# Kernel optimization log

Measured on AMD Instinct MI355X. Metric: run time of the kernel, lower is better.

Reference implementation:

```python
import jax, jax.numpy as jnp
import numpy as np
import math

EMBED_DIM = 512
NUM_HEADS = 8
HEAD_DIM = EMBED_DIM // NUM_HEADS


def setup_inputs() -> dict:
    key = jax.random.key(0)
    ks = jax.random.split(key, 11)
    s = 1.0 / math.sqrt(EMBED_DIM)
    x = jax.random.normal(ks[0], (8, EMBED_DIM, 32, 32), dtype=jnp.float32)
    Wq = jax.random.uniform(ks[1], (EMBED_DIM, EMBED_DIM), jnp.float32, -s, s)
    bq = jax.random.uniform(ks[2], (EMBED_DIM,), jnp.float32, -s, s)
    Wk = jax.random.uniform(ks[3], (EMBED_DIM, EMBED_DIM), jnp.float32, -s, s)
    bk = jax.random.uniform(ks[4], (EMBED_DIM,), jnp.float32, -s, s)
    Wv = jax.random.uniform(ks[5], (EMBED_DIM, EMBED_DIM), jnp.float32, -s, s)
    bv = jax.random.uniform(ks[6], (EMBED_DIM,), jnp.float32, -s, s)
    Wo = jax.random.uniform(ks[7], (EMBED_DIM, EMBED_DIM), jnp.float32, -s, s)
    bo = jax.random.uniform(ks[8], (EMBED_DIM,), jnp.float32, -s, s)
    gamma = jnp.ones((EMBED_DIM,), jnp.float32)
    beta = jnp.zeros((EMBED_DIM,), jnp.float32)
    return {"x": x, "Wq": Wq, "bq": bq, "Wk": Wk, "bk": bk, "Wv": Wv,
            "bv": bv, "Wo": Wo, "bo": bo, "gamma": gamma, "beta": beta}


def layer_norm(x, gamma, beta, eps=1e-5):
    mu = jnp.mean(x, axis=-1, keepdims=True)
    var = jnp.mean(jnp.square(x - mu), axis=-1, keepdims=True)
    return (x - mu) * jax.lax.rsqrt(var + eps) * gamma + beta


def reference(x, Wq, bq, Wk, bk, Wv, bv, Wo, bo, gamma, beta):
    B, C, H, W = x.shape
    S = H * W
    # [B, S, C]
    x_flat = x.reshape(B, C, S).transpose(0, 2, 1)
    residual = x_flat
    xn = layer_norm(x_flat, gamma, beta)
    # torch Linear: y = x @ W^T + b
    q = (xn @ Wq.T + bq).reshape(B, S, NUM_HEADS, HEAD_DIM)
    k = (xn @ Wk.T + bk).reshape(B, S, NUM_HEADS, HEAD_DIM)
    v = (xn @ Wv.T + bv).reshape(B, S, NUM_HEADS, HEAD_DIM)
    scale = 1.0 / math.sqrt(HEAD_DIM)
    scores = jnp.einsum('bqhd,bkhd->bhqk', q, k) * scale
    attn = jax.nn.softmax(scores, axis=-1)  # dropout is identity in eval
    out = jnp.einsum('bhqk,bkhd->bqhd', attn, v).reshape(B, S, C)
    out = out @ Wo.T + bo + residual
    return out.transpose(0, 2, 1).reshape(B, C, H, W)
```

## Files before the change

### kernel.cpp

```cpp
#include <hip/hip_runtime.h>
#include <hip/hip_bf16.h>

typedef __bf16 bf16_t;
typedef __bf16 bf16x8 __attribute__((ext_vector_type(8)));
typedef float floatx4 __attribute__((ext_vector_type(4)));

#define EMBED 512
#define S_LEN 1024
#define NH 8
#define HD 64
#define LDK 1056
#define LDV 1088

#define MFMA16(a, b, c) __builtin_amdgcn_mfma_f32_16x16x32_bf16(a, b, c, 0, 0, 0)

static __device__ __forceinline__ bf16_t f2bf(float f) {
    unsigned int x = __builtin_bit_cast(unsigned int, f);
    unsigned int lsb = (x >> 16) & 1u;
    x += 0x7fffu + lsb;
    unsigned short u = (unsigned short)(x >> 16);
    return __builtin_bit_cast(bf16_t, u);
}
static __device__ __forceinline__ float bf2f(bf16_t v) {
    unsigned short u = __builtin_bit_cast(unsigned short, v);
    unsigned int x = ((unsigned int)u) << 16;
    return __builtin_bit_cast(float, x);
}
static __device__ __forceinline__ unsigned int pack2(float lo, float hi) {
    return (__builtin_bit_cast(unsigned int, lo) >> 16) |
           (__builtin_bit_cast(unsigned int, hi) & 0xFFFF0000u);
}
static __device__ __forceinline__ unsigned int pack2r(float lo, float hi) {
    unsigned short a = __builtin_bit_cast(unsigned short, f2bf(lo));
    unsigned short b = __builtin_bit_cast(unsigned short, f2bf(hi));
    return (unsigned int)a | ((unsigned int)b << 16);
}

__global__ __launch_bounds__(256) void cvt4_kernel(const float* __restrict__ s0,
                                                   const float* __restrict__ s1,
                                                   const float* __restrict__ s2,
                                                   const float* __restrict__ s3,
                                                   bf16_t* __restrict__ d0,
                                                   bf16_t* __restrict__ d1,
                                                   bf16_t* __restrict__ d2,
                                                   bf16_t* __restrict__ d3) {
    const float* s; bf16_t* d;
    switch (blockIdx.y) {
        case 0:  s = s0; d = d0; break;
        case 1:  s = s1; d = d1; break;
        case 2:  s = s2; d = d2; break;
        default: s = s3; d = d3; break;
    }
    int i = (blockIdx.x * 256 + threadIdx.x) * 8;
#pragma unroll
    for (int j = 0; j < 8; ++j) d[i + j] = f2bf(s[i + j]);
}

__global__ __launch_bounds__(256) void ln_fused_kernel(const float* __restrict__ x,
                                                       const float* __restrict__ gamma,
                                                       const float* __restrict__ beta,
                                                       bf16_t* __restrict__ xn) {
    __shared__ float T[32][521];
    __shared__ float Pm[32][33], Pq[32][33];
    __shared__ float Mu[32], Rs[32];
    int bid = blockIdx.x;
    int b = bid >> 5, s0 = (bid & 31) * 32;
    int t = threadIdx.x;
    int lc = t >> 3;
    int si = (t & 7) * 4;
    const float* xp = x + ((size_t)b * EMBED + lc) * S_LEN + s0 + si;
    float sm[4] = {}, sq[4] = {};
#pragma unroll
    for (int p = 0; p < 16; ++p) {
        int c = lc + p * 32;
        float4 v = *(const float4*)(xp + (size_t)p * 32 * S_LEN);
        int cs = c ^ ((c >> 3) & 0x38);
        T[si + 0][cs] = v.x; T[si + 1][cs] = v.y;
        T[si + 2][cs] = v.z; T[si + 3][cs] = v.w;
        sm[0] += v.x; sq[0] += v.x * v.x;
        sm[1] += v.y; sq[1] += v.y * v.y;
        sm[2] += v.z; sq[2] += v.z * v.z;
        sm[3] += v.w; sq[3] += v.w * v.w;
    }
#pragma unroll
    for (int k = 0; k < 4; ++k) { Pm[si + k][lc] = sm[k]; Pq[si + k][lc] = sq[k]; }
    __syncthreads();
    if (t < 32) {
        float m = 0.f, q = 0.f;
#pragma unroll
        for (int j = 0; j < 32; ++j) { m += Pm[t][j]; q += Pq[t][j]; }
        float mu = m * (1.0f / EMBED);
        float var = q * (1.0f / EMBED) - mu * mu;
        Mu[t] = mu; Rs[t] = rsqrtf(var + 1e-5f);
    }
    __syncthreads();
    int cidx = t & 31;
    int rw = t >> 5;
#pragma unroll
    for (int rg = 0; rg < 4; ++rg) {
        int srl = rg * 8 + rw;
        float mu = Mu[srl], rs = Rs[srl];
        int cb = cidx * 16;
        bf16_t* dst = xn + ((size_t)b * S_LEN + s0 + srl) * EMBED + cb;
#pragma unroll
        for (int h = 0; h < 2; ++h) {
            int c0h = cb + h * 8;
            float4 g0 = *(const float4*)(gamma + c0h);
            float4 g1 = *(const float4*)(gamma + c0h + 4);
            float4 be0 = *(const float4*)(beta + c0h);
            float4 be1 = *(const float4*)(beta + c0h + 4);
            float gv[8] = {g0.x, g0.y, g0.z, g0.w, g1.x, g1.y, g1.z, g1.w};
            float bv[8] = {be0.x, be0.y, be0.z, be0.w, be1.x, be1.y, be1.z, be1.w};
            bf16x8 o;
#pragma unroll
            for (int j = 0; j < 8; ++j) {
                int c = c0h + j;
                int cs = c ^ ((c >> 3) & 0x38);
                o[j] = f2bf((T[srl][cs] - mu) * rs * gv[j] + bv[j]);
            }
            *(bf16x8*)(dst + h * 8) = o;
        }
    }
}

__global__ __launch_bounds__(256) void gemm_kernel(const bf16_t* __restrict__ X,
                                                   const bf16_t* __restrict__ W,
                                                   const float* __restrict__ b0,
                                                   const float* __restrict__ b1,
                                                   const float* __restrict__ b2,
                                                   bf16_t* __restrict__ Y,
                                                   bf16_t* __restrict__ vtb) {
    __shared__ __align__(16) bf16_t Wl[2][128 * 72];
    int t = threadIdx.x;
    int col0 = blockIdx.y * 128, row0 = blockIdx.x * 128;
    int scol = t >> 1, sseg = (t & 1) * 32;
    const bf16_t* wsrc = W + (size_t)(col0 + scol) * EMBED + sseg;
    {
        bf16x8 r0 = *(const bf16x8*)(wsrc);
        bf16x8 r1 = *(const bf16x8*)(wsrc + 8);
        bf16x8 r2 = *(const bf16x8*)(wsrc + 16);
        bf16x8 r3 = *(const bf16x8*)(wsrc + 24);
        bf16_t* d = &Wl[0][scol * 72 + sseg];
        *(bf16x8*)d = r0;        *(bf16x8*)(d + 8) = r1;
        *(bf16x8*)(d + 16) = r2; *(bf16x8*)(d + 24) = r3;
    }
    int lane = t & 63, w = t >> 6, g = lane >> 4, n16 = lane & 15;
    int rw0 = row0 + w * 32;
    const bf16_t* xr0 = X + (size_t)(rw0 + n16) * EMBED + g * 8;
    const bf16_t* xr1 = xr0 + (size_t)16 * EMBED;
    bf16x8 a00 = *(const bf16x8*)(xr0);
    bf16x8 a01 = *(const bf16x8*)(xr0 + 32);
    bf16x8 a10 = *(const bf16x8*)(xr1);
    bf16x8 a11 = *(const bf16x8*)(xr1 + 32);
    __syncthreads();
    floatx4 acc[2][8] = {};
#pragma unroll
    for (int kc = 0; kc < 8; ++kc) {
        bf16x8 p0, p1, p2, p3, na00, na01, na10, na11;
        if (kc < 7) {
            int ko = (kc + 1) * 64;
            p0 = *(const bf16x8*)(wsrc + ko);
            p1 = *(const bf16x8*)(wsrc + ko + 8);
            p2 = *(const bf16x8*)(wsrc + ko + 16);
            p3 = *(const bf16x8*)(wsrc + ko + 24);
            na00 = *(const bf16x8*)(xr0 + ko);
            na01 = *(const bf16x8*)(xr0 + ko + 32);
            na10 = *(const bf16x8*)(xr1 + ko);
            na11 = *(const bf16x8*)(xr1 + ko + 32);
        }
        const bf16_t* wl = &Wl[kc & 1][0];
#pragma unroll
        for (int kk = 0; kk < 2; ++kk) {
            bf16x8 s0 = (kk == 0) ? a00 : a01;
            bf16x8 s1 = (kk == 0) ? a10 : a11;
#pragma unroll
            for (int nt = 0; nt < 8; ++nt) {
                bf16x8 bfr = *(const bf16x8*)(&wl[(nt * 16 + n16) * 72 + kk * 32 + g * 8]);
                acc[0][nt] = MFMA16(s0, bfr, acc[0][nt]);
                acc[1][nt] = MFMA16(s1, bfr, acc[1][nt]);
            }
        }
        if (kc < 7) {
            bf16_t* d = &Wl[(kc + 1) & 1][scol * 72 + sseg];
            *(bf16x8*)d = p0;        *(bf16x8*)(d + 8) = p1;
            *(bf16x8*)(d + 16) = p2; *(bf16x8*)(d + 24) = p3;
            a00 = na00; a01 = na01; a10 = na10; a11 = na11;
        }
        __syncthreads();
    }
    if (col0 < 1024) {
        const float* bp = (col0 < 512) ? b0 : b1;
#pragma unroll
        for (int ar = 0; ar < 2; ++ar)
#pragma unroll
            for (int nt = 0; nt < 8; ++nt) {
                int col = col0 + nt * 16 + n16;
                float bv = bp[col & 511];
#pragma unroll
                for (int r = 0; r < 4; ++r) {
                    int row = rw0 + ar * 16 + g * 4 + r;
                    Y[(size_t)row * LDK + col] = f2bf(acc[ar][nt][r] + bv);
                }
            }
    } else {
        bf16_t* Tl = &Wl[0][0];
#pragma unroll
        for (int ar = 0; ar < 2; ++ar)
#pragma unroll
            for (int nt = 0; nt < 8; ++nt) {
                int chl = nt * 16 + n16;
                float bv = b2[(col0 & 511) + chl];
                uint2 pr;
                pr.x = pack2r(acc[ar][nt][0] + bv, acc[ar][nt][1] + bv);
                pr.y = pack2r(acc[ar][nt][2] + bv, acc[ar][nt][3] + bv);
                *(uint2*)(&Tl[chl * 136 + w * 32 + ar * 16 + g * 4]) = pr;
            }
        __syncthreads();
        int ch = t >> 1, seg = (t & 1) * 64;
        int bb = row0 >> 10, s0 = row0 & 1023;
        bf16_t* dst = vtb + ((size_t)(bb * EMBED + (col0 - 1024) + ch)) * LDV + s0 + seg;
        const bf16_t* srcl = &Tl[ch * 136 + seg];
#pragma unroll
        for (int i = 0; i < 8; ++i)
            *(bf16x8*)(dst + i * 8) = *(const bf16x8*)(srcl + i * 8);
    }
}

__global__ __launch_bounds__(256) void wsgemm_out_kernel(const bf16_t* __restrict__ Wb,
                                                         const bf16_t* __restrict__ act,
                                                         const float* __restrict__ bias,
                                                         const float* __restrict__ xres,
                                                         float* __restrict__ out) {
    __shared__ __align__(16) bf16_t Al[2][64 * 72];
    int b = blockIdx.z, n0 = blockIdx.x * 64, m0 = blockIdx.y * 128;
    int t = threadIdx.x;
    int srow = t >> 2, sseg = (t & 3) * 16;
    const bf16_t* asrc = act + ((size_t)b * S_LEN + n0 + srow) * EMBED + sseg;
    {
        bf16x8 r0 = *(const bf16x8*)(asrc);
        bf16x8 r1 = *(const bf16x8*)(asrc + 8);
        bf16_t* d = &Al[0][srow * 72 + sseg];
        *(bf16x8*)d = r0; *(bf16x8*)(d + 8) = r1;
    }
    int lane = t & 63, w = t >> 6, g = lane >> 4, n16 = lane & 15;
    int mw = m0 + w * 32;
    const bf16_t* wr0 = Wb + (size_t)(mw + n16) * EMBED + g * 8;
    const bf16_t* wr1 = wr0 + (size_t)16 * EMBED;
    bf16x8 a00 = *(const bf16x8*)(wr0);
    bf16x8 a01 = *(const bf16x8*)(wr0 + 32);
    bf16x8 a10 = *(const bf16x8*)(wr1);
    bf16x8 a11 = *(const bf16x8*)(wr1 + 32);
    __syncthreads();
    floatx4 acc[2][4] = {};
#pragma unroll
    for (int kc = 0; kc < 8; ++kc) {
        bf16x8 p0, p1, na00, na01, na10, na11;
        if (kc < 7) {
            int ko = (kc + 1) * 64;
            p0 = *(const bf16x8*)(asrc + ko);
            p1 = *(const bf16x8*)(asrc + ko + 8);
            na00 = *(const bf16x8*)(wr0 + ko);
            na01 = *(const bf16x8*)(wr0 + ko + 32);
            na10 = *(const bf16x8*)(wr1 + ko);
            na11 = *(const bf16x8*)(wr1 + ko + 32);
        }
        const bf16_t* al = &Al[kc & 1][0];
#pragma unroll
        for (int kk = 0; kk < 2; ++kk) {
            bf16x8 s0 = (kk == 0) ? a00 : a01;
            bf16x8 s1 = (kk == 0) ? a10 : a11;
#pragma unroll
            for (int nt = 0; nt < 4; ++nt) {
                bf16x8 bfr = *(const bf16x8*)(&al[(nt * 16 + n16) * 72 + kk * 32 + g * 8]);
                acc[0][nt] = MFMA16(s0, bfr, acc[0][nt]);
                acc[1][nt] = MFMA16(s1, bfr, acc[1][nt]);
            }
        }
        if (kc < 7) {
            bf16_t* d = &Al[(kc + 1) & 1][srow * 72 + sseg];
            *(bf16x8*)d = p0; *(bf16x8*)(d + 8) = p1;
            a00 = na00; a01 = na01; a10 = na10; a11 = na11;
        }
        __syncthreads();
    }
#pragma unroll
    for (int ar = 0; ar < 2; ++ar)
#pragma unroll
        for (int r = 0; r < 4; ++r) {
            int row = mw + ar * 16 + g * 4 + r;
            float bv = bias[row];
#pragma unroll
            for (int nt = 0; nt < 4; ++nt) {
                int col = n0 + nt * 16 + n16;
                size_t oi = ((size_t)b * EMBED + row) * S_LEN + col;
                out[oi] = acc[ar][nt][r] + bv + xres[oi];
            }
        }
}

__global__ __launch_bounds__(256) void attn_kernel(const bf16_t* __restrict__ qk,
                                                   const bf16_t* __restrict__ vt,
                                                   bf16_t* __restrict__ o) {
    __shared__ __align__(16) bf16_t Kt[2][64 * 72];
    __shared__ __align__(16) bf16_t Vl2[2][64 * 72];
    __shared__ __align__(16) unsigned int Pl[4][16 * 36];
    int bid = blockIdx.x;
    int bh = bid & 63, qt = bid >> 6;
    int b = bh >> 3, h = bh & 7;
    int t = threadIdx.x, w = t >> 6, lane = t & 63, g = lane >> 4, n16 = lane & 15;
    size_t baseQK = (size_t)b * S_LEN * LDK;
    size_t baseV  = ((size_t)b * EMBED + h * HD) * LDV;
    int qA = qt * 128 + w * 32 + n16;

    const bf16_t* qpA = qk + baseQK + (size_t)qA * LDK + h * HD + g * 8;
    const bf16_t* qpB = qpA + (size_t)16 * LDK;
    bf16x8 qa0 = *(const bf16x8*)(qpA);
    bf16x8 qa1 = *(const bf16x8*)(qpA + 32);
    bf16x8 qb0 = *(const bf16x8*)(qpB);
    bf16x8 qb1 = *(const bf16x8*)(qpB + 32);
#pragma unroll
    for (int j = 0; j < 8; ++j) {
        qa0[j] = f2bf(bf2f(qa0[j]) * 0.125f);
        qa1[j] = f2bf(bf2f(qa1[j]) * 0.125f);
        qb0[j] = f2bf(bf2f(qb0[j]) * 0.125f);
        qb1[j] = f2bf(bf2f(qb1[j]) * 0.125f);
    }
    const bf16_t* kbase = qk + baseQK + 512 + h * HD;
    const bf16_t* vbase = vt + baseV;

    int srow = t >> 2, scol = (t & 3) * 16;
    const bf16_t* ksrc = kbase + (size_t)srow * LDK + scol;
    const bf16_t* vsrc = vbase + (size_t)srow * LDV + scol;
    {
        bf16x8 k0 = *(const bf16x8*)(ksrc);
        bf16x8 k1 = *(const bf16x8*)(ksrc + 8);
        bf16x8 v0 = *(const bf16x8*)(vsrc);
        bf16x8 v1 = *(const bf16x8*)(vsrc + 8);
        bf16_t* kd = &Kt[0][srow * 72 + scol];
        bf16_t* vd = &Vl2[0][srow * 72 + scol];
        *(bf16x8*)kd = k0; *(bf16x8*)(kd + 8) = k1;
        *(bf16x8*)vd = v0; *(bf16x8*)(vd + 8) = v1;
    }

    float lsA[4] = {}, lsB[4] = {};
    floatx4 oaccA[4] = {}, oaccB[4] = {};
    unsigned int* PLw = &Pl[w][0];

    for (int it = 0; it < 16; ++it) {
        int cur = it & 1, nxt = cur ^ 1;
        __syncthreads();
        bf16x8 pk0, pk1, pv0, pv1;
        if (it < 15) {
            const bf16_t* kp = ksrc + (size_t)(it + 1) * 64 * LDK;
            pk0 = *(const bf16x8*)(kp);
            pk1 = *(const bf16x8*)(kp + 8);
            const bf16_t* vp = vsrc + (it + 1) * 64;
            pv0 = *(const bf16x8*)(vp);
            pv1 = *(const bf16x8*)(vp + 8);
        }
        const bf16_t* Kl = &Kt[cur][0];
        const bf16_t* Vl = &Vl2[cur][0];
        floatx4 sA[4], sB[4];
#pragma unroll
        for (int kb = 0; kb < 4; ++kb) {
            bf16x8 k0 = *(const bf16x8*)(&Kl[(kb * 16 + n16) * 72 + g * 8]);
            bf16x8 k1 = *(const bf16x8*)(&Kl[(kb * 16 + n16) * 72 + 32 + g * 8]);
            sA[kb] = floatx4{-12.f, -12.f, -12.f, -12.f};
            sA[kb] = MFMA16(k0, qa0, sA[kb]);
            sA[kb] = MFMA16(k1, qa1, sA[kb]);
            sB[kb] = floatx4{-12.f, -12.f, -12.f, -12.f};
            sB[kb] = MFMA16(k0, qb0, sB[kb]);
            sB[kb] = MFMA16(k1, qb1, sB[kb]);
        }
        if (it < 15) {
            bf16_t* kd = &Kt[nxt][srow * 72 + scol];
            bf16_t* vd = &Vl2[nxt][srow * 72 + scol];
            *(bf16x8*)kd = pk0; *(bf16x8*)(kd + 8) = pk1;
            *(bf16x8*)vd = pv0; *(bf16x8*)(vd + 8) = pv1;
        }
#pragma unroll
        for (int kb = 0; kb < 4; ++kb)
#pragma unroll
            for (int r = 0; r < 4; ++r) {
                float eA = __expf(fminf(sA[kb][r], 40.f));
                sA[kb][r] = eA; lsA[kb] += eA;
                float eB = __expf(fminf(sB[kb][r], 40.f));
                sB[kb][r] = eB; lsB[kb] += eB;
            }
#pragma unroll
        for (int kb = 0; kb < 4; ++kb) {
            uint2 pr;
            pr.x = pack2(sA[kb][0], sA[kb][1]);
            pr.y = pack2(sA[kb][2], sA[kb][3]);
            *(uint2*)&PLw[n16 * 36 + kb * 8 + g * 2] = pr;
        }
        uint4 uA0 = *(const uint4*)&PLw[n16 * 36 + g * 4];
        uint4 uA1 = *(const uint4*)&PLw[n16 * 36 + 16 + g * 4];
        bf16x8 pfA0 = __builtin_bit_cast(bf16x8, uA0);
        bf16x8 pfA1 = __builtin_bit_cast(bf16x8, uA1);
#pragma unroll
        for (int kb = 0; kb < 4; ++kb) {
            uint2 pr;
            pr.x = pack2(sB[kb][0], sB[kb][1]);
            pr.y = pack2(sB[kb][2], sB[kb][3]);
            *(uint2*)&PLw[n16 * 36 + kb * 8 + g * 2] = pr;
        }
        uint4 uB0 = *(const uint4*)&PLw[n16 * 36 + g * 4];
        uint4 uB1 = *(const uint4*)&PLw[n16 * 36 + 16 + g * 4];
        bf16x8 pfB0 = __builtin_bit_cast(bf16x8, uB0);
        bf16x8 pfB1 = __builtin_bit_cast(bf16x8, uB1);
#pragma unroll
        for (int dt = 0; dt < 4; ++dt) {
            bf16x8 v0 = *(const bf16x8*)(&Vl[(dt * 16 + n16) * 72 + g * 8]);
            bf16x8 v1 = *(const bf16x8*)(&Vl[(dt * 16 + n16) * 72 + 32 + g * 8]);
            oaccA[dt] = MFMA16(v0, pfA0, oaccA[dt]);
            oaccA[dt] = MFMA16(v1, pfA1, oaccA[dt]);
            oaccB[dt] = MFMA16(v0, pfB0, oaccB[dt]);
            oaccB[dt] = MFMA16(v1, pfB1, oaccB[dt]);
        }
    }
    float lA = (lsA[0] + lsA[1]) + (lsA[2] + lsA[3]);
    lA += __shfl_xor(lA, 16);
    lA += __shfl_xor(lA, 32);
    float lB = (lsB[0] + lsB[1]) + (lsB[2] + lsB[3]);
    lB += __shfl_xor(lB, 16);
    lB += __shfl_xor(lB, 32);
    float rlA = 1.0f / lA, rlB = 1.0f / lB;
    size_t orowA = ((size_t)b * S_LEN + qA) * EMBED + h * HD;
    size_t orowB = orowA + (size_t)16 * EMBED;
#pragma unroll
    for (int dt = 0; dt < 4; ++dt) {
        uint2 prA, prB;
        prA.x = pack2(oaccA[dt][0] * rlA, oaccA[dt][1] * rlA);
        prA.y = pack2(oaccA[dt][2] * rlA, oaccA[dt][3] * rlA);
        *(uint2*)(o + orowA + dt * 16 + g * 4) = prA;
        prB.x = pack2(oaccB[dt][0] * rlB, oaccB[dt][1] * rlB);
        prB.y = pack2(oaccB[dt][2] * rlB, oaccB[dt][3] * rlB);
        *(uint2*)(o + orowB + dt * 16 + g * 4) = prB;
    }
}

extern "C" void kernel_launch(void* const* d_in, const int* in_sizes, int n_in,
                              void* d_out, int out_size, void* d_ws, size_t ws_size,
                              hipStream_t stream) {
    const float* x     = (const float*)d_in[0];
    const float* Wq    = (const float*)d_in[1];
    const float* bq    = (const float*)d_in[2];
    const float* Wk    = (const float*)d_in[3];
    const float* bk    = (const float*)d_in[4];
    const float* Wv    = (const float*)d_in[5];
    const float* bv    = (const float*)d_in[6];
    const float* Wo    = (const float*)d_in[7];
    const float* bo    = (const float*)d_in[8];
    const float* gamma = (const float*)d_in[9];
    const float* beta  = (const float*)d_in[10];
    float* out = (float*)d_out;

    char* ws = (char*)d_ws;
    bf16_t* xn    = (bf16_t*)ws;
    bf16_t* qkb   = (bf16_t*)(ws + 8388608);
    bf16_t* wqkv  = (bf16_t*)(ws + 25690112);
    bf16_t* wo    = (bf16_t*)(ws + 27262976);
    bf16_t* ab    = xn;

    bf16_t* vtb = (bf16_t*)d_out;

    cvt4_kernel<<<dim3(128, 4), 256, 0, stream>>>(Wq, Wk, Wv, Wo,
                                                  wqkv, wqkv + 262144,
                                                  wqkv + 524288, wo);
    ln_fused_kernel<<<dim3(256), 256, 0, stream>>>(x, gamma, beta, xn);
    gemm_kernel<<<dim3(64, 12), 256, 0, stream>>>(xn, wqkv, bq, bk, bv, qkb, vtb);
    attn_kernel<<<dim3(512), 256, 0, stream>>>(qkb, vtb, ab);
    wsgemm_out_kernel<<<dim3(16, 4, 8), 256, 0, stream>>>(wo, ab, bo, x, out);
}
```

Before: 167.4 us.

## Load V fragments directly from global, use exp2 softmax, add MFMA priority hints

Measured after the change: 176.3 us. 1.05x slower.

```diff
diff --git a/kernel.cpp b/kernel.cpp
--- a/kernel.cpp
+++ b/kernel.cpp
@@ -302,7 +302,6 @@
                                                    const bf16_t* __restrict__ vt,
                                                    bf16_t* __restrict__ o) {
     __shared__ __align__(16) bf16_t Kt[2][64 * 72];
-    __shared__ __align__(16) bf16_t Vl2[2][64 * 72];
     __shared__ __align__(16) unsigned int Pl[4][16 * 36];
     int bid = blockIdx.x;
     int bh = bid & 63, qt = bid >> 6;
@@ -312,6 +311,7 @@
     size_t baseV  = ((size_t)b * EMBED + h * HD) * LDV;
     int qA = qt * 128 + w * 32 + n16;
 
+    const float QSC = 0.18033688f;
     const bf16_t* qpA = qk + baseQK + (size_t)qA * LDK + h * HD + g * 8;
     const bf16_t* qpB = qpA + (size_t)16 * LDK;
     bf16x8 qa0 = *(const bf16x8*)(qpA);
@@ -320,71 +320,71 @@
     bf16x8 qb1 = *(const bf16x8*)(qpB + 32);
 #pragma unroll
     for (int j = 0; j < 8; ++j) {
-        qa0[j] = f2bf(bf2f(qa0[j]) * 0.125f);
-        qa1[j] = f2bf(bf2f(qa1[j]) * 0.125f);
-        qb0[j] = f2bf(bf2f(qb0[j]) * 0.125f);
-        qb1[j] = f2bf(bf2f(qb1[j]) * 0.125f);
+        qa0[j] = f2bf(bf2f(qa0[j]) * QSC);
+        qa1[j] = f2bf(bf2f(qa1[j]) * QSC);
+        qb0[j] = f2bf(bf2f(qb0[j]) * QSC);
+        qb1[j] = f2bf(bf2f(qb1[j]) * QSC);
     }
     const bf16_t* kbase = qk + baseQK + 512 + h * HD;
     const bf16_t* vbase = vt + baseV;
 
     int srow = t >> 2, scol = (t & 3) * 16;
     const bf16_t* ksrc = kbase + (size_t)srow * LDK + scol;
-    const bf16_t* vsrc = vbase + (size_t)srow * LDV + scol;
     {
         bf16x8 k0 = *(const bf16x8*)(ksrc);
         bf16x8 k1 = *(const bf16x8*)(ksrc + 8);
-        bf16x8 v0 = *(const bf16x8*)(vsrc);
-        bf16x8 v1 = *(const bf16x8*)(vsrc + 8);
         bf16_t* kd = &Kt[0][srow * 72 + scol];
-        bf16_t* vd = &Vl2[0][srow * 72 + scol];
         *(bf16x8*)kd = k0; *(bf16x8*)(kd + 8) = k1;
-        *(bf16x8*)vd = v0; *(bf16x8*)(vd + 8) = v1;
     }
 
     float lsA[4] = {}, lsB[4] = {};
     floatx4 oaccA[4] = {}, oaccB[4] = {};
     unsigned int* PLw = &Pl[w][0];
+    const float NEG12L2E = -17.3123405f;
+    const float CLAMP    =  57.7078018f;
 
     for (int it = 0; it < 16; ++it) {
         int cur = it & 1, nxt = cur ^ 1;
         __syncthreads();
-        bf16x8 pk0, pk1, pv0, pv1;
+        bf16x8 vf0[4], vf1[4];
+#pragma unroll
+        for (int dt = 0; dt < 4; ++dt) {
+            const bf16_t* vp = vbase + (size_t)(dt * 16 + n16) * LDV + it * 64 + g * 8;
+            vf0[dt] = *(const bf16x8*)(vp);
+            vf1[dt] = *(const bf16x8*)(vp + 32);
+        }
+        bf16x8 pk0, pk1;
         if (it < 15) {
             const bf16_t* kp = ksrc + (size_t)(it + 1) * 64 * LDK;
             pk0 = *(const bf16x8*)(kp);
             pk1 = *(const bf16x8*)(kp + 8);
-            const bf16_t* vp = vsrc + (it + 1) * 64;
-            pv0 = *(const bf16x8*)(vp);
-            pv1 = *(const bf16x8*)(vp + 8);
         }
         const bf16_t* Kl = &Kt[cur][0];
-        const bf16_t* Vl = &Vl2[cur][0];
         floatx4 sA[4], sB[4];
+        __builtin_amdgcn_s_setprio(1);
 #pragma unroll
         for (int kb = 0; kb < 4; ++kb) {
             bf16x8 k0 = *(const bf16x8*)(&Kl[(kb * 16 + n16) * 72 + g * 8]);
             bf16x8 k1 = *(const bf16x8*)(&Kl[(kb * 16 + n16) * 72 + 32 + g * 8]);
-            sA[kb] = floatx4{-12.f, -12.f, -12.f, -12.f};
+            sA[kb] = floatx4{NEG12L2E, NEG12L2E, NEG12L2E, NEG12L2E};
             sA[kb] = MFMA16(k0, qa0, sA[kb]);
             sA[kb] = MFMA16(k1, qa1, sA[kb]);
-            sB[kb] = floatx4{-12.f, -12.f, -12.f, -12.f};
+            sB[kb] = floatx4{NEG12L2E, NEG12L2E, NEG12L2E, NEG12L2E};
             sB[kb] = MFMA16(k0, qb0, sB[kb]);
             sB[kb] = MFMA16(k1, qb1, sB[kb]);
         }
+        __builtin_amdgcn_s_setprio(0);
         if (it < 15) {
             bf16_t* kd = &Kt[nxt][srow * 72 + scol];
-            bf16_t* vd = &Vl2[nxt][srow * 72 + scol];
             *(bf16x8*)kd = pk0; *(bf16x8*)(kd + 8) = pk1;
-            *(bf16x8*)vd = pv0; *(bf16x8*)(vd + 8) = pv1;
         }
 #pragma unroll
         for (int kb = 0; kb < 4; ++kb)
 #pragma unroll
             for (int r = 0; r < 4; ++r) {
-                float eA = __expf(fminf(sA[kb][r], 40.f));
+                float eA = exp2f(fminf(sA[kb][r], CLAMP));
                 sA[kb][r] = eA; lsA[kb] += eA;
-                float eB = __expf(fminf(sB[kb][r], 40.f));
+                float eB = exp2f(fminf(sB[kb][r], CLAMP));
                 sB[kb][r] = eB; lsB[kb] += eB;
             }
 #pragma unroll
@@ -409,15 +409,15 @@
         uint4 uB1 = *(const uint4*)&PLw[n16 * 36 + 16 + g * 4];
         bf16x8 pfB0 = __builtin_bit_cast(bf16x8, uB0);
         bf16x8 pfB1 = __builtin_bit_cast(bf16x8, uB1);
+        __builtin_amdgcn_s_setprio(1);
 #pragma unroll
         for (int dt = 0; dt < 4; ++dt) {
-            bf16x8 v0 = *(const bf16x8*)(&Vl[(dt * 16 + n16) * 72 + g * 8]);
-            bf16x8 v1 = *(const bf16x8*)(&Vl[(dt * 16 + n16) * 72 + 32 + g * 8]);
-            oaccA[dt] = MFMA16(v0, pfA0, oaccA[dt]);
-            oaccA[dt] = MFMA16(v1, pfA1, oaccA[dt]);
-            oaccB[dt] = MFMA16(v0, pfB0, oaccB[dt]);
-            oaccB[dt] = MFMA16(v1, pfB1, oaccB[dt]);
-        }
+            oaccA[dt] = MFMA16(vf0[dt], pfA0, oaccA[dt]);
+            oaccA[dt] = MFMA16(vf1[dt], pfA1, oaccA[dt]);
+            oaccB[dt] = MFMA16(vf0[dt], pfB0, oaccB[dt]);
+            oaccB[dt] = MFMA16(vf1[dt], pfB1, oaccB[dt]);
+        }
+        __builtin_amdgcn_s_setprio(0);
     }
     float lA = (lsA[0] + lsA[1]) + (lsA[2] + lsA[3]);
     lA += __shfl_xor(lA, 16);
```
